# Kernel optimization log

Measured on AMD Instinct MI355X. Metric: run time of the kernel, lower is better.

Reference implementation:

```python
import jax, jax.numpy as jnp
import numpy as np
from jax import lax

silu = jax.nn.silu

def conv2d(x, w, b, pad):
    y = lax.conv_general_dilated(x, w, (1, 1), [(pad, pad), (pad, pad)],
                                 dimension_numbers=('NCHW', 'OIHW', 'NCHW'))
    return y + b[None, :, None, None]

def avgpool2(x):
    B, C, H, W = x.shape
    return x.reshape(B, C, H // 2, 2, W // 2, 2).mean(axis=(3, 5))

def up2x(x):
    # bilinear scale_factor=2, align_corners=True (matches F.interpolate)
    B, C, H, W = x.shape
    Ho, Wo = 2 * H, 2 * W
    ys = jnp.arange(Ho, dtype=x.dtype) * ((H - 1) / (Ho - 1))
    xs = jnp.arange(Wo, dtype=x.dtype) * ((W - 1) / (Wo - 1))
    y0 = jnp.floor(ys).astype(jnp.int32); y1 = jnp.minimum(y0 + 1, H - 1); wy = ys - y0
    x0 = jnp.floor(xs).astype(jnp.int32); x1 = jnp.minimum(x0 + 1, W - 1); wx = xs - x0
    row = x[:, :, y0, :] * (1 - wy)[None, None, :, None] + x[:, :, y1, :] * wy[None, None, :, None]
    return row[:, :, :, x0] * (1 - wx) + row[:, :, :, x1] * wx

def deform_conv2d(x, offset, weight, groups):
    # torchvision DeformConv2d semantics: stride=1, pad=(k-1)//2, dilation=1, no bias
    B, Cin, H, W = x.shape
    Cout, cpg, kh, kw = weight.shape  # cpg = Cin // groups
    K = kh * kw
    OG = offset.shape[1] // (2 * K)   # offset groups
    Cog = Cin // OG
    off = offset.reshape(B, OG, K, 2, H, W)  # (dy, dx) per kernel tap
    ki = jnp.repeat(jnp.arange(kh, dtype=x.dtype) - (kh - 1) // 2, kw)  # [K]
    kj = jnp.tile(jnp.arange(kw, dtype=x.dtype) - (kw - 1) // 2, kh)
    py = off[:, :, :, 0] + jnp.arange(H, dtype=x.dtype)[None, None, None, :, None] + ki[None, None, :, None, None]
    px = off[:, :, :, 1] + jnp.arange(W, dtype=x.dtype)[None, None, None, None, :] + kj[None, None, :, None, None]
    y0f = jnp.floor(py); x0f = jnp.floor(px)
    ly = py - y0f; lx = px - x0f
    y0 = y0f.astype(jnp.int32); x0 = x0f.astype(jnp.int32)
    xg = x.reshape(B, OG, Cog, H * W)

    def corner(yi, xi, wt):
        valid = (yi >= 0) & (yi < H) & (xi >= 0) & (xi < W)
        idx = jnp.clip(yi, 0, H - 1) * W + jnp.clip(xi, 0, W - 1)        # [B,OG,K,H,W]
        idxf = jnp.broadcast_to(idx.reshape(B, OG, 1, K * H * W), (B, OG, Cog, K * H * W))
        v = jnp.take_along_axis(xg, idxf, axis=3).reshape(B, OG, Cog, K, H, W)
        return v * (wt * valid)[:, :, None]

    val = (corner(y0, x0, (1 - ly) * (1 - lx)) + corner(y0, x0 + 1, (1 - ly) * lx)
           + corner(y0 + 1, x0, ly * (1 - lx)) + corner(y0 + 1, x0 + 1, ly * lx))
    # grouped contraction over sampled taps
    valg = val.reshape(B, groups, Cin // groups, K, H, W)
    wg = weight.reshape(groups, Cout // groups, cpg, K)
    return jnp.einsum('bgckhw,gock->bgohw', valg, wg).reshape(B, Cout, H, W)

def setup_inputs() -> dict:
    key = jax.random.key(0)
    ks = iter(jax.random.split(key, 64))
    def w(shape, s=0.05):
        return jax.random.normal(next(ks), shape, jnp.float32) * s
    B, H, W = 4, 512, 512
    d = {'x': jax.random.normal(next(ks), (B, 4, H, W), jnp.float32)}
    # offset estimators (small scale so sampled offsets stay moderate)
    d['eo1_w1'] = w((18, 4, 5, 5), 0.02);  d['eo1_b1'] = w((18,), 0.02)
    d['eo1_w2'] = w((36, 18, 5, 5), 0.02); d['eo1_b2'] = w((36,), 0.02)
    d['dcw1'] = w((2, 2, 3, 3))            # DeformConv2d(4->2, groups=2)
    d['c1d_w1'] = w((4, 2, 3, 3));   d['c1d_b1'] = w((4,))
    d['c1d_w2'] = w((8, 4, 3, 3));   d['c1d_b2'] = w((8,))
    d['eo2_w1'] = w((18, 8, 5, 5), 0.02);  d['eo2_b1'] = w((18,), 0.02)
    d['eo2_w2'] = w((36, 18, 5, 5), 0.02); d['eo2_b2'] = w((36,), 0.02)
    d['dcw2'] = w((8, 4, 3, 3))            # DeformConv2d(8->8, groups=2)
    d['c2d_w1'] = w((12, 8, 3, 3));  d['c2d_b1'] = w((12,))
    d['c2d_w2'] = w((16, 12, 3, 3)); d['c2d_b2'] = w((16,))
    d['eo3_w1'] = w((18, 16, 5, 5), 0.02); d['eo3_b1'] = w((18,), 0.02)
    d['eo3_w2'] = w((36, 18, 5, 5), 0.02); d['eo3_b2'] = w((36,), 0.02)
    d['dcw3'] = w((16, 8, 3, 3))           # DeformConv2d(16->16, groups=2)
    d['c3d_w1'] = w((14, 16, 3, 3)); d['c3d_b1'] = w((14,))
    d['c3d_w2'] = w((12, 14, 3, 3)); d['c3d_b2'] = w((12,))
    d['up2_w'] = w((12, 12, 3, 3));  d['up2_b'] = w((12,))
    d['c2u_w1'] = w((16, 28, 3, 3)); d['c2u_b1'] = w((16,))
    d['c2u_w2'] = w((8, 16, 3, 3));  d['c2u_b2'] = w((8,))
    d['up1_w'] = w((8, 8, 3, 3));    d['up1_b'] = w((8,))
    d['c1u_w1'] = w((8, 16, 3, 3));  d['c1u_b1'] = w((8,))
    d['c1u_w2'] = w((2, 8, 3, 3));   d['c1u_b2'] = w((2,))
    return d

def reference(x, eo1_w1, eo1_b1, eo1_w2, eo1_b2, dcw1, c1d_w1, c1d_b1, c1d_w2, c1d_b2,
              eo2_w1, eo2_b1, eo2_w2, eo2_b2, dcw2, c2d_w1, c2d_b1, c2d_w2, c2d_b2,
              eo3_w1, eo3_b1, eo3_w2, eo3_b2, dcw3, c3d_w1, c3d_b1, c3d_w2, c3d_b2,
              up2_w, up2_b, c2u_w1, c2u_b1, c2u_w2, c2u_b2, up1_w, up1_b,
              c1u_w1, c1u_b1, c1u_w2, c1u_b2):
    def convbasic(h, w1, b1, w2, b2):
        return silu(conv2d(silu(conv2d(h, w1, b1, 1)), w2, b2, 1))
    # level 1 down
    off1 = conv2d(conv2d(x, eo1_w1, eo1_b1, 2), eo1_w2, eo1_b2, 2)
    comp1 = deform_conv2d(x, off1, dcw1, groups=2)
    conv1_d = convbasic(comp1, c1d_w1, c1d_b1, c1d_w2, c1d_b2)
    pool1 = avgpool2(conv1_d)
    # level 2 down
    off2 = conv2d(conv2d(pool1, eo2_w1, eo2_b1, 2), eo2_w2, eo2_b2, 2)
    comp2 = deform_conv2d(pool1, off2, dcw2, groups=2)
    conv2_d = convbasic(comp2, c2d_w1, c2d_b1, c2d_w2, c2d_b2)
    pool2 = avgpool2(conv2_d)
    # level 3 (bottleneck)
    off3 = conv2d(conv2d(pool2, eo3_w1, eo3_b1, 2), eo3_w2, eo3_b2, 2)
    comp3 = deform_conv2d(pool2, off3, dcw3, groups=2)
    conv3_d = convbasic(comp3, c3d_w1, c3d_b1, c3d_w2, c3d_b2)
    # up path
    usmpl2 = silu(conv2d(up2x(conv3_d), up2_w, up2_b, 1))
    conv2_u = convbasic(jnp.concatenate([usmpl2, conv2_d], axis=1), c2u_w1, c2u_b1, c2u_w2, c2u_b2)
    usmpl1 = silu(conv2d(up2x(conv2_u), up1_w, up1_b, 1))
    conv1_u = convbasic(jnp.concatenate([usmpl1, conv1_d], axis=1), c1u_w1, c1u_b1, c1u_w2, c1u_b2)
    return conv1_u
```

## Files before the change

### kernel.cpp

```cpp
#include <hip/hip_runtime.h>
#include <math.h>

#define THREADS 256
typedef __attribute__((ext_vector_type(2))) float f32x2;
typedef __attribute__((ext_vector_type(4))) float f32x4;

__device__ __forceinline__ float silu_f(float v) {
    return v / (1.f + __expf(-v));
}

__device__ __forceinline__ void pk_fma_lo(f32x2& d, f32x2 a, f32x2 b) {
    asm("v_pk_fma_f32 %0, %1, %2, %0 op_sel:[0,0,0] op_sel_hi:[0,1,1]"
        : "+v"(d) : "v"(a), "v"(b));
}
__device__ __forceinline__ void pk_fma_hi(f32x2& d, f32x2 a, f32x2 b) {
    asm("v_pk_fma_f32 %0, %1, %2, %0 op_sel:[1,0,0] op_sel_hi:[1,1,1]"
        : "+v"(d) : "v"(a), "v"(b));
}

struct TEnt { const float* src; int dst; int cin; int cout; int k2; int base; int n; };
struct TTab { TEnt e[40]; int total; };

__global__ __launch_bounds__(THREADS)
void transpose_w_k(TTab t, float* __restrict__ tw) {
    const int i = blockIdx.x * THREADS + threadIdx.x;
    if (i >= t.total) return;
    int j = 0;
    while (i >= t.e[j].base + t.e[j].n) ++j;
    const TEnt e = t.e[j];
    const int local = i - e.base;
    const int co  = local % e.cout;
    const int tmp = local / e.cout;
    const int k   = tmp % e.k2;
    const int ci  = tmp / e.k2;
    tw[e.dst + local] = e.src[(co * e.cin + ci) * e.k2 + k];
}

template<int KS, int PX>
__device__ __forceinline__ void load_row(float* __restrict__ rr,
                                         const float* __restrict__ rp,
                                         bool vy, int x0, int W)
{
    constexpr int PAD = (KS - 1) / 2;
    constexpr int RW = PX + KS - 1;
#pragma unroll
    for (int q = -1; q <= PX / 4; ++q) {
        if (4 * q + 3 + PAD < 0 || 4 * q + PAD >= RW) continue;
        const int xs = x0 + 4 * q;
        constexpr bool SAFE_Q = false;
        (void)SAFE_Q;
        const bool safe = (q >= 0) && (4 * q + 3 < PX);
        float vc[4] = {0.f, 0.f, 0.f, 0.f};
        if (safe) {
            if (vy) {
                const float4 v = *reinterpret_cast<const float4*>(rp + xs);
                vc[0] = v.x; vc[1] = v.y; vc[2] = v.z; vc[3] = v.w;
            }
        } else if (vy && xs >= 0 && xs + 4 <= W) {
            const float4 v = *reinterpret_cast<const float4*>(rp + xs);
            vc[0] = v.x; vc[1] = v.y; vc[2] = v.z; vc[3] = v.w;
        } else if (vy) {
#pragma unroll
            for (int c = 0; c < 4; ++c)
                vc[c] = ((unsigned)(xs + c) < (unsigned)W) ? rp[xs + c] : 0.f;
        }
#pragma unroll
        for (int c = 0; c < 4; ++c) {
            const int t = 4 * q + c + PAD;
            if (t >= 0 && t < RW) rr[t] = vc[c];
        }
    }
}

template<int CIN, int COUT, int KS, int PX, int PHASE, int RW2, int WQ, int NP>
__device__ __forceinline__ void chan_body(
    const float* __restrict__ ip0, const float* __restrict__ sw,
    int cl, int y, int x0, int W, int H, int lw, int total,
    f32x2 (&r2)[2][RW2], f32x4 (&wb)[2][WQ], f32x2 (&acc)[NP][PX])
{
    constexpr int PAD = (KS - 1) / 2;
    constexpr int K2 = KS * KS;
    constexpr int CO_S = (COUT + 3) & ~3;
#pragma unroll
    for (int ky = 0; ky < KS; ++ky) {
        {
            const bool last = (ky + 1 == KS);
            const int ncl = cl + (last ? 1 : 0);
            const int nky = last ? 0 : (ky + 1);
            if (!last || ncl < CIN) {
                const int yy = y + nky - PAD;
                load_row<KS, PX>((float*)r2[(PHASE + ky + 1) & 1],
                                 ip0 + (size_t)ncl * total + (yy << lw),
                                 (unsigned)yy < (unsigned)H, x0, W);
            }
        }
#pragma unroll
        for (int kx = 0; kx < KS; ++kx) {
            const int t = ky * KS + kx;
            const int wc = (PHASE + t) & 1;
            if (t + 1 < K2 || cl + 1 < CIN) {
                const f32x4* __restrict__ nx =
                    (const f32x4*)(sw + (size_t)(cl * K2 + t + 1) * CO_S);
#pragma unroll
                for (int q = 0; q < WQ; ++q) wb[wc ^ 1][q] = nx[q];
            }
#pragma unroll
            for (int q = 0; q < WQ; ++q) {
                const f32x4 w4 = wb[wc][q];
                const f32x2 wlo = __builtin_shufflevector(w4, w4, 0, 1);
                const f32x2 whi = __builtin_shufflevector(w4, w4, 2, 3);
#pragma unroll
                for (int s = 0; s < 2; ++s) {
                    const int p = 2 * q + s;
                    if (p < NP) {
                        const f32x2 wp = s ? whi : wlo;
#pragma unroll
                        for (int j = 0; j < PX; ++j) {
                            const int e = kx + j;
                            if (e & 1) pk_fma_hi(acc[p][j], r2[(PHASE + ky) & 1][e >> 1], wp);
                            else       pk_fma_lo(acc[p][j], r2[(PHASE + ky) & 1][e >> 1], wp);
                        }
                    }
                }
            }
            __builtin_amdgcn_sched_barrier(0);
        }
    }
}

template<int CIN, int COUT, int KS, bool ACT, int PX>
__global__ __launch_bounds__(THREADS)
void conv_sl_k(const float* __restrict__ in, const float* __restrict__ wt,
               const float* __restrict__ bias, float* __restrict__ out,
               int H, int lw, int bs_in, int bs_out, int nb, int nz)
{
    constexpr int PAD = (KS - 1) / 2;
    constexpr int K2 = KS * KS;
    constexpr int CO_S = (COUT + 3) & ~3;
    constexpr int WQ = CO_S / 4;
    constexpr int NP = COUT / 2;
    constexpr int RW = PX + KS - 1;
    constexpr int RW2 = (RW + 1) / 2;
    static_assert(CIN % 2 == 0 && COUT % 2 == 0 && PX % 4 == 0, "");
    __shared__ float sw[CIN * K2 * CO_S];

    const int lin = blockIdx.x;
    const int r8 = lin & 7;
    int q = lin >> 3;
    const int z = q % nz; q /= nz;
    const int g = q * 8 + r8;
    const int b = g % nb;
    const int xb = g / nb;

    const float* __restrict__ wz = wt + (size_t)z * (CIN * K2 * COUT);
    const int W = 1 << lw;
    const int total = H << lw;
    const int idx = (xb * THREADS + threadIdx.x) * PX;
    const float* ip0 = in + (size_t)b * bs_in;
    float* op = out + (size_t)b * bs_out + (size_t)z * COUT * total;
    const int x0 = idx & (W - 1);
    const int y  = idx >> lw;

    for (int i = threadIdx.x; i < CIN * K2 * COUT; i += THREADS)
        sw[(i / COUT) * CO_S + i % COUT] = wz[i];
    __syncthreads();

    f32x2 acc[NP][PX];
#pragma unroll
    for (int p = 0; p < NP; ++p) {
        f32x2 bb;
        bb.x = bias[z * COUT + 2 * p];
        bb.y = bias[z * COUT + 2 * p + 1];
#pragma unroll
        for (int j = 0; j < PX; ++j) acc[p][j] = bb;
    }

    f32x2 r2[2][RW2];
    f32x4 wb[2][WQ];
    {
        const int yy = y - PAD;
        load_row<KS, PX>((float*)r2[0], ip0 + (yy << lw),
                         (unsigned)yy < (unsigned)H, x0, W);
        const f32x4* __restrict__ w0 = (const f32x4*)sw;
#pragma unroll
        for (int q2 = 0; q2 < WQ; ++q2) wb[0][q2] = w0[q2];
    }

#pragma unroll 1
    for (int c2 = 0; c2 < CIN / 2; ++c2) {
        chan_body<CIN, COUT, KS, PX, 0, RW2, WQ, NP>(ip0, sw, 2 * c2,     y, x0, W, H, lw, total, r2, wb, acc);
        chan_body<CIN, COUT, KS, PX, 1, RW2, WQ, NP>(ip0, sw, 2 * c2 + 1, y, x0, W, H, lw, total, r2, wb, acc);
    }

#pragma unroll
    for (int p = 0; p < NP; ++p) {
#pragma unroll
        for (int h = 0; h < 2; ++h) {
            const int co = 2 * p + h;
#pragma unroll
            for (int j4 = 0; j4 < PX / 4; ++j4) {
                float4 v;
                float a0 = h ? acc[p][4 * j4 + 0].y : acc[p][4 * j4 + 0].x;
                float a1 = h ? acc[p][4 * j4 + 1].y : acc[p][4 * j4 + 1].x;
                float a2 = h ? acc[p][4 * j4 + 2].y : acc[p][4 * j4 + 2].x;
                float a3 = h ? acc[p][4 * j4 + 3].y : acc[p][4 * j4 + 3].x;
                v.x = ACT ? silu_f(a0) : a0;
                v.y = ACT ? silu_f(a1) : a1;
                v.z = ACT ? silu_f(a2) : a2;
                v.w = ACT ? silu_f(a3) : a3;
                *reinterpret_cast<float4*>(op + (size_t)co * total + idx + 4 * j4) = v;
            }
        }
    }
}

template<int CIN, int COUT, int KS, bool ACT, int PX>
__global__ __launch_bounds__(THREADS)
void conv_k(const float* __restrict__ in, const float* __restrict__ wt,
            const float* __restrict__ bias, float* __restrict__ out,
            int H, int lw, int bs_in, int bs_out)
{
    constexpr int PAD = (KS - 1) / 2;
    constexpr int K2 = KS * KS;
    constexpr int CO_S = (COUT + 3) & ~3;
    constexpr int WQ = CO_S / 4;
    constexpr int NP = COUT / 2;
    constexpr int RW = PX + KS - 1;
    constexpr int RW2 = (RW + 1) / 2;
    static_assert(COUT % 2 == 0, "");
    __shared__ float sw[CIN * K2 * CO_S];

    const int W = 1 << lw;
    const int total = H << lw;
    const int idx = (blockIdx.x * THREADS + threadIdx.x) * PX;
    const float* ip0 = in + (size_t)blockIdx.y * bs_in;
    float* op = out + (size_t)blockIdx.y * bs_out;
    const int x0 = idx & (W - 1);
    const int y  = idx >> lw;

    for (int i = threadIdx.x; i < CIN * K2 * COUT; i += THREADS)
        sw[(i / COUT) * CO_S + i % COUT] = wt[i];
    __syncthreads();

    f32x2 acc[NP][PX];
#pragma unroll
    for (int p = 0; p < NP; ++p) {
        f32x2 bb;
        bb.x = bias[2 * p];
        bb.y = bias[2 * p + 1];
#pragma unroll
        for (int j = 0; j < PX; ++j) acc[p][j] = bb;
    }

#pragma unroll 1
    for (int cl = 0; cl < CIN; ++cl) {
        const float* __restrict__ row0 = ip0 + (size_t)cl * total;
        f32x2 r2[KS][RW2];
#pragma unroll
        for (int ky = 0; ky < KS; ++ky) {
            const int yy = y + ky - PAD;
            load_row<KS, PX>((float*)r2[ky], row0 + (yy << lw),
                             (unsigned)yy < (unsigned)H, x0, W);
        }
        const float* __restrict__ wbase = &sw[cl * K2 * CO_S];
#pragma unroll
        for (int t = 0; t < K2; ++t) {
            const int ky = t / KS, kx = t % KS;
            const f32x4* __restrict__ wv = (const f32x4*)(wbase + t * CO_S);
#pragma unroll
            for (int q = 0; q < WQ; ++q) {
                const f32x4 w4 = wv[q];
                const f32x2 wlo = __builtin_shufflevector(w4, w4, 0, 1);
                const f32x2 whi = __builtin_shufflevector(w4, w4, 2, 3);
#pragma unroll
                for (int s = 0; s < 2; ++s) {
                    const int p = 2 * q + s;
                    if (p < NP) {
                        const f32x2 wp = s ? whi : wlo;
#pragma unroll
                        for (int j = 0; j < PX; ++j) {
                            const int e = kx + j;
                            if (e & 1) pk_fma_hi(acc[p][j], r2[ky][e >> 1], wp);
                            else       pk_fma_lo(acc[p][j], r2[ky][e >> 1], wp);
                        }
                    }
                }
            }
            __builtin_amdgcn_sched_barrier(0);
        }
    }

#pragma unroll
    for (int p = 0; p < NP; ++p) {
#pragma unroll
        for (int h = 0; h < 2; ++h) {
            const int co = 2 * p + h;
            if (PX == 2) {
                float2 v;
                float a0 = h ? acc[p][0].y : acc[p][0].x;
                float a1 = h ? acc[p][1].y : acc[p][1].x;
                v.x = ACT ? silu_f(a0) : a0;
                v.y = ACT ? silu_f(a1) : a1;
                *reinterpret_cast<float2*>(op + (size_t)co * total + idx) = v;
            } else {
#pragma unroll
                for (int j4 = 0; j4 < PX / 4; ++j4) {
                    float4 v;
                    float a0 = h ? acc[p][4 * j4 + 0].y : acc[p][4 * j4 + 0].x;
                    float a1 = h ? acc[p][4 * j4 + 1].y : acc[p][4 * j4 + 1].x;
                    float a2 = h ? acc[p][4 * j4 + 2].y : acc[p][4 * j4 + 2].x;
                    float a3 = h ? acc[p][4 * j4 + 3].y : acc[p][4 * j4 + 3].x;
                    v.x = ACT ? silu_f(a0) : a0;
                    v.y = ACT ? silu_f(a1) : a1;
                    v.z = ACT ? silu_f(a2) : a2;
                    v.w = ACT ? silu_f(a3) : a3;
                    *reinterpret_cast<float4*>(op + (size_t)co * total + idx + 4 * j4) = v;
                }
            }
        }
    }
}

template<int CIN, int COUT>
__global__ __launch_bounds__(THREADS)
void dconv_k(const float* __restrict__ in, const float* __restrict__ off,
             const float* __restrict__ twg0, const float* __restrict__ twg1,
             float* __restrict__ out,
             int H, int lw, int bs_in, int bs_off, int bs_out)
{
    constexpr int K = 9;
    constexpr int OG = 2;
    constexpr int COG = CIN / OG;
    constexpr int COUTG = COUT / 2;
    constexpr int NWG = COG * K * COUTG;
    __shared__ float sw[2 * NWG];
    for (int i = threadIdx.x; i < 2 * NWG; i += THREADS)
        sw[i] = (i < NWG) ? twg0[i] : twg1[i - NWG];
    __syncthreads();

    const int W = 1 << lw;
    const int total = H << lw;
    const int idx = blockIdx.x * THREADS + threadIdx.x;
    const float* ip0 = in + (size_t)blockIdx.y * bs_in;
    const float* offp = off + (size_t)blockIdx.y * bs_off;
    float* op = out + (size_t)blockIdx.y * bs_out;
    const int x = idx & (W - 1);
    const int y = idx >> lw;

    float acc[COUT];
#pragma unroll
    for (int co = 0; co < COUT; ++co) acc[co] = 0.f;

#pragma unroll
    for (int og = 0; og < OG; ++og) {
#pragma unroll
        for (int k = 0; k < K; ++k) {
            const int ki = k / 3 - 1;
            const int kj = k % 3 - 1;
            const float dy = offp[(size_t)(((og * K + k) * 2 + 0)) * total + idx];
            const float dx = offp[(size_t)(((og * K + k) * 2 + 1)) * total + idx];
            const float py = dy + (float)(y + ki);
            const float px = dx + (float)(x + kj);
            const float y0f = floorf(py), x0f = floorf(px);
            const float ly = py - y0f, lx = px - x0f;
            const int y0 = (int)y0f, x0 = (int)x0f;
            const int y1 = y0 + 1, x1 = x0 + 1;
            const bool vy0 = (unsigned)y0 < (unsigned)H;
            const bool vy1 = (unsigned)y1 < (unsigned)H;
            const bool vx0 = (unsigned)x0 < (unsigned)W;
            const bool vx1 = (unsigned)x1 < (unsigned)W;
            const int cy0 = min(max(y0, 0), H - 1), cy1 = min(max(y1, 0), H - 1);
            const int cx0 = min(max(x0, 0), W - 1), cx1 = min(max(x1, 0), W - 1);
            const int i00 = (cy0 << lw) + cx0, i01 = (cy0 << lw) + cx1;
            const int i10 = (cy1 << lw) + cx0, i11 = (cy1 << lw) + cx1;
            const float f00 = (vy0 && vx0) ? (1.f - ly) * (1.f - lx) : 0.f;
            const float f01 = (vy0 && vx1) ? (1.f - ly) * lx : 0.f;
            const float f10 = (vy1 && vx0) ? ly * (1.f - lx) : 0.f;
            const float f11 = (vy1 && vx1) ? ly * lx : 0.f;
            const float* swg = &sw[og * NWG];
#pragma unroll
            for (int c = 0; c < COG; ++c) {
                const float* __restrict__ ip = ip0 + (size_t)(og * COG + c) * total;
                const float v = f00 * ip[i00] + f01 * ip[i01]
                              + f10 * ip[i10] + f11 * ip[i11];
                const float* __restrict__ wr = &swg[(c * K + k) * COUTG];
#pragma unroll
                for (int col = 0; col < COUTG; ++col)
                    acc[og * COUTG + col] = fmaf(v, wr[col], acc[og * COUTG + col]);
            }
        }
    }

#pragma unroll
    for (int co = 0; co < COUT; ++co)
        op[(size_t)co * total + idx] = acc[co];
}

__global__ __launch_bounds__(THREADS)
void avgpool_k(const float* __restrict__ in, float* __restrict__ out,
               int n, int lt, int lwo, int bsi, int bso)
{
    const int idx = blockIdx.x * THREADS + threadIdx.x;
    if (idx >= n) return;
    const float* ip0 = in + (size_t)blockIdx.y * bsi;
    float* op = out + (size_t)blockIdx.y * bso;
    const int c = idx >> lt;
    const int r = idx & ((1 << lt) - 1);
    const int oy = r >> lwo;
    const int ox = r & ((1 << lwo) - 1);
    const int Wi = 2 << lwo;
    const float* ip = ip0 + ((size_t)c << (lt + 2)) + ((size_t)(2 * oy) << (lwo + 1)) + 2 * ox;
    const float2 t = *reinterpret_cast<const float2*>(ip);
    const float2 b = *reinterpret_cast<const float2*>(ip + Wi);
    op[idx] = 0.25f * (t.x + t.y + b.x + b.y);
}

__global__ __launch_bounds__(THREADS)
void up2x_k(const float* __restrict__ in, float* __restrict__ out,
            int n, int lt, int lwo, int Hin, int bsi, int bso)
{
    const int idx = blockIdx.x * THREADS + threadIdx.x;
    if (idx >= n) return;
    const float* ip0 = in + (size_t)blockIdx.y * bsi;
    float* op = out + (size_t)blockIdx.y * bso;
    const int c = idx >> lt;
    const int r = idx & ((1 << lt) - 1);
    const int oy = r >> lwo;
    const int ox = r & ((1 << lwo) - 1);
    const int W = 1 << (lwo - 1);
    const int H = Hin;
    const float s = (float)(H - 1) / (float)(2 * H - 1);
    const float fy = (float)oy * s;
    const float fx = (float)ox * s;
    const int y0 = (int)fy;
    const int x0 = (int)fx;
    const int y1 = min(y0 + 1, H - 1);
    const int x1 = min(x0 + 1, W - 1);
    const float wy = fy - (float)y0;
    const float wx = fx - (float)x0;
    const float* ip = ip0 + ((size_t)c << (lt - 2));
    const float v00 = ip[y0 * W + x0], v01 = ip[y0 * W + x1];
    const float v10 = ip[y1 * W + x0], v11 = ip[y1 * W + x1];
    op[idx] = (v00 * (1.f - wy) + v10 * wy) * (1.f - wx)
            + (v01 * (1.f - wy) + v11 * wy) * wx;
}

__global__ __launch_bounds__(THREADS)
void copy_k(float4* __restrict__ dst, const float4* __restrict__ src,
            int n4, int bsd, int bss)
{
    const int i = blockIdx.x * THREADS + threadIdx.x;
    if (i >= n4) return;
    dst[(size_t)blockIdx.y * bsd + i] = src[(size_t)blockIdx.y * bss + i];
}


extern "C" void kernel_launch(void* const* d_in, const int* in_sizes, int n_in,
                              void* d_out, int out_size, void* d_ws, size_t ws_size,
                              hipStream_t stream) {
    const float* x      = (const float*)d_in[0];
    const float* eo1_b1 = (const float*)d_in[2];
    const float* eo1_b2 = (const float*)d_in[4];
    const float* c1d_b1 = (const float*)d_in[7];
    const float* c1d_b2 = (const float*)d_in[9];
    const float* eo2_b1 = (const float*)d_in[11];
    const float* eo2_b2 = (const float*)d_in[13];
    const float* c2d_b1 = (const float*)d_in[16];
    const float* c2d_b2 = (const float*)d_in[18];
    const float* eo3_b1 = (const float*)d_in[20];
    const float* eo3_b2 = (const float*)d_in[22];
    const float* c3d_b1 = (const float*)d_in[25];
    const float* c3d_b2 = (const float*)d_in[27];
    const float* up2_b  = (const float*)d_in[29];
    const float* c2u_b1 = (const float*)d_in[31];
    const float* c2u_b2 = (const float*)d_in[33];
    const float* up1_b  = (const float*)d_in[35];
    const float* c1u_b1 = (const float*)d_in[37];
    const float* c1u_b2 = (const float*)d_in[39];

    float* out = (float*)d_out;
    float* wsf = (float*)d_ws;

    constexpr int H1 = 512, A1 = H1 * H1;
    constexpr int H2 = 256, A2 = H2 * H2;
    constexpr int H3 = 128, A3 = H3 * H3;
    constexpr int TW_FLOATS = 81920;
    constexpr int SLOT = 58 * A1;

    const int widx[34]  = {1, 1, 1,  3, 3, 3, 3, 3,  6, 8,
                           10, 10, 10,  12, 12, 12, 12, 12,  15, 17,
                           19,  21, 21, 21, 21, 21,  24, 26,
                           28, 30, 32, 34, 36, 38};
    const int wcin[34]  = {4, 4, 4,  18, 18, 18, 18, 18,  2, 4,
                           8, 8, 8,  18, 18, 18, 18, 18,  8, 12,
                           16,  18, 18, 18, 18, 18,  16, 14,
                           12, 28, 16, 8, 16, 8};
    const int wcout[34] = {6, 6, 6,  8, 8, 8, 8, 4,  4, 8,
                           6, 6, 6,  8, 8, 8, 8, 4,  12, 16,
                           18,  8, 8, 8, 8, 4,  14, 12,
                           12, 16, 8, 8, 8, 2};
    const int wk2[34]   = {25, 25, 25,  25, 25, 25, 25, 25,  9, 9,
                           25, 25, 25,  25, 25, 25, 25, 25,  9, 9,
                           25,  25, 25, 25, 25, 25,  9, 9,
                           9, 9, 9, 9, 9, 9};
    const int wsoff[34] = {0, 600, 1200,  0, 3600, 7200, 10800, 14400,  0, 0,
                           0, 1200, 2400,  0, 3600, 7200, 10800, 14400,  0, 0,
                           0,  0, 3600, 7200, 10800, 14400,  0, 0,
                           0, 0, 0, 0, 0, 0};
    const int cont[34]  = {1, 1, 0,  1, 1, 1, 0, 0,  0, 0,
                           1, 1, 0,  1, 1, 1, 0, 0,  0, 0,
                           0,  1, 1, 1, 0, 0,  0, 0,
                           0, 0, 0, 0, 0, 0};
    TTab tab;
    const float* tw[40];
    int off = 0, base = 0;
    for (int i = 0; i < 34; ++i) {
        const int n = wcin[i] * wcout[i] * wk2[i];
        tab.e[i].src = (const float*)d_in[widx[i]] + wsoff[i];
        tab.e[i].dst = off; tab.e[i].cin = wcin[i]; tab.e[i].cout = wcout[i];
        tab.e[i].k2 = wk2[i]; tab.e[i].base = base; tab.e[i].n = n;
        tw[i] = wsf + off;
        off = cont[i] ? (off + n) : ((off + n + 63) & ~63);
        base += n;
    }
    const int didx[3]   = {5, 14, 23};
    const int dcoutg[3] = {1, 4, 8};
    const int dcpg[3]   = {2, 4, 8};
    for (int i = 0; i < 3; ++i) {
        for (int g = 0; g < 2; ++g) {
            const int e = 34 + 2 * i + g;
            const int n = dcoutg[i] * dcpg[i] * 9;
            tab.e[e].src = (const float*)d_in[didx[i]] + (size_t)g * n;
            tab.e[e].dst = off; tab.e[e].cin = dcpg[i]; tab.e[e].cout = dcoutg[i];
            tab.e[e].k2 = 9; tab.e[e].base = base; tab.e[e].n = n;
            tw[e] = wsf + off;
            off = (off + n + 63) & ~63;
            base += n;
        }
    }
    tab.total = base;
    transpose_w_k<<<(base + THREADS - 1) / THREADS, THREADS, 0, stream>>>(tab, wsf);

    int B = 4;
    while (B > 1 && ws_size < ((size_t)TW_FLOATS + (size_t)B * SLOT) * sizeof(float)) B >>= 1;

    auto run_all = [&](int Bc, float* slot, int SB,
                       const float* xin, int xbs, float* outp, int obs) {
        float* S0 = slot;
        float* S1 = S0 + 36 * A1;
        float* S2 = S1 + 18 * A1;
        float* P  = S2 + 2 * A1;
        float* L1 = S1 + 10 * A1;
        float* L2 = S0 + 32 * A1;
        auto gs = [&](int n, int px, int z) { return dim3((n / (px * THREADS)) * Bc * z); };
        auto gp = [&](int n, int px) { return dim3(n / (px * THREADS), Bc); };
        auto g1 = [&](int n) { return dim3((n + THREADS - 1) / THREADS, Bc); };

        conv_sl_k<4, 6, 5, false, 8><<<gs(A1, 8, 3), THREADS, 0, stream>>>(xin, tw[0], eo1_b1, S1, H1, 9, xbs, SB, Bc, 3);
        conv_sl_k<18, 8, 5, false, 8><<<gs(A1, 8, 4), THREADS, 0, stream>>>(S1, tw[3], eo1_b2, S0, H1, 9, SB, SB, Bc, 4);
        conv_sl_k<18, 4, 5, false, 8><<<gs(A1, 8, 1), THREADS, 0, stream>>>(S1, tw[7], eo1_b2 + 32, S0 + 32 * A1, H1, 9, SB, SB, Bc, 1);
        dconv_k<4, 2><<<g1(A1), THREADS, 0, stream>>>(xin, S0, tw[34], tw[35], S2, H1, 9, xbs, SB, SB);
        conv_k<2, 4, 3, true, 8><<<gp(A1, 8), THREADS, 0, stream>>>(S2, tw[8], c1d_b1, S1, H1, 9, SB, SB);
        conv_k<4, 8, 3, true, 8><<<gp(A1, 8), THREADS, 0, stream>>>(S1, tw[9], c1d_b2, L1, H1, 9, SB, SB);
        avgpool_k<<<g1(8 * A2), THREADS, 0, stream>>>(L1, P, 8 * A2, 16, 8, SB, SB);

        conv_sl_k<8, 6, 5, false, 8><<<gs(A2, 8, 3), THREADS, 0, stream>>>(P, tw[10], eo2_b1, S1, H2, 8, SB, SB, Bc, 3);
        conv_sl_k<18, 8, 5, false, 8><<<gs(A2, 8, 4), THREADS, 0, stream>>>(S1, tw[13], eo2_b2, S0, H2, 8, SB, SB, Bc, 4);
        conv_sl_k<18, 4, 5, false, 8><<<gs(A2, 8, 1), THREADS, 0, stream>>>(S1, tw[17], eo2_b2 + 32, S0 + 32 * A2, H2, 8, SB, SB, Bc, 1);
        dconv_k<8, 8><<<g1(A2), THREADS, 0, stream>>>(P, S0, tw[36], tw[37], S2, H2, 8, SB, SB, SB);
        conv_k<8, 12, 3, true, 4><<<gp(A2, 4), THREADS, 0, stream>>>(S2, tw[18], c2d_b1, S1, H2, 8, SB, SB);
        conv_k<12, 16, 3, true, 4><<<gp(A2, 4), THREADS, 0, stream>>>(S1, tw[19], c2d_b2, L2, H2, 8, SB, SB);
        avgpool_k<<<g1(16 * A3), THREADS, 0, stream>>>(L2, P, 16 * A3, 14, 7, SB, SB);

        conv_k<16, 18, 5, false, 2><<<gp(A3, 2), THREADS, 0, stream>>>(P, tw[20], eo3_b1, S1, H3, 7, SB, SB);
        conv_sl_k<18, 8, 5, false, 4><<<gs(A3, 4, 4), THREADS, 0, stream>>>(S1, tw[21], eo3_b2, S0, H3, 7, SB, SB, Bc, 4);
        conv_sl_k<18, 4, 5, false, 4><<<gs(A3, 4, 1), THREADS, 0, stream>>>(S1, tw[25], eo3_b2 + 32, S0 + 32 * A3, H3, 7, SB, SB, Bc, 1);
        dconv_k<16, 16><<<g1(A3), THREADS, 0, stream>>>(P, S0, tw[38], tw[39], S2, H3, 7, SB, SB, SB);
        conv_k<16, 14, 3, true, 2><<<gp(A3, 2), THREADS, 0, stream>>>(S2, tw[26], c3d_b1, S1, H3, 7, SB, SB);
        conv_k<14, 12, 3, true, 2><<<gp(A3, 2), THREADS, 0, stream>>>(S1, tw[27], c3d_b2, S2, H3, 7, SB, SB);

        up2x_k<<<g1(12 * A2), THREADS, 0, stream>>>(S2, S0, 12 * A2, 16, 8, H3, SB, SB);
        conv_k<12, 12, 3, true, 4><<<gp(A2, 4), THREADS, 0, stream>>>(S0, tw[28], up2_b, S1, H2, 8, SB, SB);
        copy_k<<<g1(4 * A2), THREADS, 0, stream>>>((float4*)(S1 + 12 * A2), (const float4*)L2,
                                                   4 * A2, SB / 4, SB / 4);
        conv_k<28, 16, 3, true, 4><<<gp(A2, 4), THREADS, 0, stream>>>(S1, tw[29], c2u_b1, S0, H2, 8, SB, SB);
        conv_k<16, 8, 3, true, 4><<<gp(A2, 4), THREADS, 0, stream>>>(S0, tw[30], c2u_b2, S2, H2, 8, SB, SB);

        up2x_k<<<g1(8 * A1), THREADS, 0, stream>>>(S2, S0, 8 * A1, 18, 9, H2, SB, SB);
        conv_k<8, 8, 3, true, 8><<<gp(A1, 8), THREADS, 0, stream>>>(S0, tw[31], up1_b, S0 + 8 * A1, H1, 9, SB, SB);
        copy_k<<<g1(2 * A1), THREADS, 0, stream>>>((float4*)(S0 + 16 * A1), (const float4*)L1,
                                                   2 * A1, SB / 4, SB / 4);
        conv_k<16, 8, 3, true, 8><<<gp(A1, 8), THREADS, 0, stream>>>(S0 + 8 * A1, tw[32], c1u_b1, S1, H1, 9, SB, SB);
        conv_k<8, 2, 3, true, 8><<<gp(A1, 8), THREADS, 0, stream>>>(S1, tw[33], c1u_b2, outp, H1, 9, SB, obs);
    };

    for (int g = 0; g < 4; g += B)
        run_all(B, wsf + TW_FLOATS, SLOT,
                x + (size_t)g * 4 * A1, 4 * A1,
                out + (size_t)g * 2 * A1, 2 * A1);
}
```

Measured before the change: 1.536 ms.

## Read conv weights via scalar loads into SGPRs instead of LDS staging

Removes the shared-memory weight staging and __syncthreads from both conv kernels. Weights are now read straight from global memory as uniform values with a double-buffered prefetch, and the packed FMA asm takes the weight operand as an SGPR. This cuts LDS traffic, VGPR pressure and the block-start barrier. In exchange it relies on the compiler emitting scalar loads and on the scalar cache holding the weights, and if it does not, the inline asm 's' constraints could force readfirstlane moves or fail to compile.

```diff
diff --git a/kernel.cpp b/kernel.cpp
--- a/kernel.cpp
+++ b/kernel.cpp
@@ -3,19 +3,18 @@
 
 #define THREADS 256
 typedef __attribute__((ext_vector_type(2))) float f32x2;
-typedef __attribute__((ext_vector_type(4))) float f32x4;
 
 __device__ __forceinline__ float silu_f(float v) {
     return v / (1.f + __expf(-v));
 }
 
-__device__ __forceinline__ void pk_fma_lo(f32x2& d, f32x2 a, f32x2 b) {
+__device__ __forceinline__ void pk_fma_lo_s(f32x2& d, f32x2 a, f32x2 b) {
     asm("v_pk_fma_f32 %0, %1, %2, %0 op_sel:[0,0,0] op_sel_hi:[0,1,1]"
-        : "+v"(d) : "v"(a), "v"(b));
-}
-__device__ __forceinline__ void pk_fma_hi(f32x2& d, f32x2 a, f32x2 b) {
+        : "+v"(d) : "v"(a), "s"(b));
+}
+__device__ __forceinline__ void pk_fma_hi_s(f32x2& d, f32x2 a, f32x2 b) {
     asm("v_pk_fma_f32 %0, %1, %2, %0 op_sel:[1,0,0] op_sel_hi:[1,1,1]"
-        : "+v"(d) : "v"(a), "v"(b));
+        : "+v"(d) : "v"(a), "s"(b));
 }
 
 struct TEnt { const float* src; int dst; int cin; int cout; int k2; int base; int n; };
@@ -47,8 +46,6 @@
     for (int q = -1; q <= PX / 4; ++q) {
         if (4 * q + 3 + PAD < 0 || 4 * q + PAD >= RW) continue;
         const int xs = x0 + 4 * q;
-        constexpr bool SAFE_Q = false;
-        (void)SAFE_Q;
         const bool safe = (q >= 0) && (4 * q + 3 < PX);
         float vc[4] = {0.f, 0.f, 0.f, 0.f};
         if (safe) {
@@ -72,15 +69,15 @@
     }
 }
 
-template<int CIN, int COUT, int KS, int PX, int PHASE, int RW2, int WQ, int NP>
+template<int CIN, int COUT, int KS, int PX, int PHASE, int RW2, int NP>
 __device__ __forceinline__ void chan_body(
-    const float* __restrict__ ip0, const float* __restrict__ sw,
+    const float* __restrict__ ip0, const float* __restrict__ wz,
     int cl, int y, int x0, int W, int H, int lw, int total,
-    f32x2 (&r2)[2][RW2], f32x4 (&wb)[2][WQ], f32x2 (&acc)[NP][PX])
+    f32x2 (&r2)[2][RW2], f32x2 (&wb)[2][NP], f32x2 (&acc)[NP][PX])
 {
     constexpr int PAD = (KS - 1) / 2;
     constexpr int K2 = KS * KS;
-    constexpr int CO_S = (COUT + 3) & ~3;
+    static_assert(K2 % 2 == 1, "parity continuity needs odd K2");
 #pragma unroll
     for (int ky = 0; ky < KS; ++ky) {
         {
@@ -99,28 +96,19 @@
             const int t = ky * KS + kx;
             const int wc = (PHASE + t) & 1;
             if (t + 1 < K2 || cl + 1 < CIN) {
-                const f32x4* __restrict__ nx =
-                    (const f32x4*)(sw + (size_t)(cl * K2 + t + 1) * CO_S);
-#pragma unroll
-                for (int q = 0; q < WQ; ++q) wb[wc ^ 1][q] = nx[q];
-            }
-#pragma unroll
-            for (int q = 0; q < WQ; ++q) {
-                const f32x4 w4 = wb[wc][q];
-                const f32x2 wlo = __builtin_shufflevector(w4, w4, 0, 1);
-                const f32x2 whi = __builtin_shufflevector(w4, w4, 2, 3);
-#pragma unroll
-                for (int s = 0; s < 2; ++s) {
-                    const int p = 2 * q + s;
-                    if (p < NP) {
-                        const f32x2 wp = s ? whi : wlo;
-#pragma unroll
-                        for (int j = 0; j < PX; ++j) {
-                            const int e = kx + j;
-                            if (e & 1) pk_fma_hi(acc[p][j], r2[(PHASE + ky) & 1][e >> 1], wp);
-                            else       pk_fma_lo(acc[p][j], r2[(PHASE + ky) & 1][e >> 1], wp);
-                        }
-                    }
+                const f32x2* __restrict__ nx =
+                    (const f32x2*)(wz + (size_t)(cl * K2 + t + 1) * COUT);
+#pragma unroll
+                for (int p = 0; p < NP; ++p) wb[wc ^ 1][p] = nx[p];
+            }
+#pragma unroll
+            for (int p = 0; p < NP; ++p) {
+                const f32x2 wp = wb[wc][p];
+#pragma unroll
+                for (int j = 0; j < PX; ++j) {
+                    const int e = kx + j;
+                    if (e & 1) pk_fma_hi_s(acc[p][j], r2[(PHASE + ky) & 1][e >> 1], wp);
+                    else       pk_fma_lo_s(acc[p][j], r2[(PHASE + ky) & 1][e >> 1], wp);
                 }
             }
             __builtin_amdgcn_sched_barrier(0);
@@ -136,13 +124,10 @@
 {
     constexpr int PAD = (KS - 1) / 2;
     constexpr int K2 = KS * KS;
-    constexpr int CO_S = (COUT + 3) & ~3;
-    constexpr int WQ = CO_S / 4;
     constexpr int NP = COUT / 2;
     constexpr int RW = PX + KS - 1;
     constexpr int RW2 = (RW + 1) / 2;
     static_assert(CIN % 2 == 0 && COUT % 2 == 0 && PX % 4 == 0, "");
-    __shared__ float sw[CIN * K2 * CO_S];
 
     const int lin = blockIdx.x;
     const int r8 = lin & 7;
@@ -161,10 +146,6 @@
     const int x0 = idx & (W - 1);
     const int y  = idx >> lw;
 
-    for (int i = threadIdx.x; i < CIN * K2 * COUT; i += THREADS)
-        sw[(i / COUT) * CO_S + i % COUT] = wz[i];
-    __syncthreads();
-
     f32x2 acc[NP][PX];
 #pragma unroll
     for (int p = 0; p < NP; ++p) {
@@ -176,20 +157,20 @@
     }
 
     f32x2 r2[2][RW2];
-    f32x4 wb[2][WQ];
+    f32x2 wb[2][NP];
     {
         const int yy = y - PAD;
         load_row<KS, PX>((float*)r2[0], ip0 + (yy << lw),
                          (unsigned)yy < (unsigned)H, x0, W);
-        const f32x4* __restrict__ w0 = (const f32x4*)sw;
-#pragma unroll
-        for (int q2 = 0; q2 < WQ; ++q2) wb[0][q2] = w0[q2];
+        const f32x2* __restrict__ w0 = (const f32x2*)wz;
+#pragma unroll
+        for (int p = 0; p < NP; ++p) wb[0][p] = w0[p];
     }
 
 #pragma unroll 1
     for (int c2 = 0; c2 < CIN / 2; ++c2) {
-        chan_body<CIN, COUT, KS, PX, 0, RW2, WQ, NP>(ip0, sw, 2 * c2,     y, x0, W, H, lw, total, r2, wb, acc);
-        chan_body<CIN, COUT, KS, PX, 1, RW2, WQ, NP>(ip0, sw, 2 * c2 + 1, y, x0, W, H, lw, total, r2, wb, acc);
+        chan_body<CIN, COUT, KS, PX, 0, RW2, NP>(ip0, wz, 2 * c2,     y, x0, W, H, lw, total, r2, wb, acc);
+        chan_body<CIN, COUT, KS, PX, 1, RW2, NP>(ip0, wz, 2 * c2 + 1, y, x0, W, H, lw, total, r2, wb, acc);
     }
 
 #pragma unroll
@@ -222,13 +203,10 @@
 {
     constexpr int PAD = (KS - 1) / 2;
     constexpr int K2 = KS * KS;
-    constexpr int CO_S = (COUT + 3) & ~3;
-    constexpr int WQ = CO_S / 4;
     constexpr int NP = COUT / 2;
     constexpr int RW = PX + KS - 1;
     constexpr int RW2 = (RW + 1) / 2;
     static_assert(COUT % 2 == 0, "");
-    __shared__ float sw[CIN * K2 * CO_S];
 
     const int W = 1 << lw;
     const int total = H << lw;
@@ -238,10 +216,6 @@
     const int x0 = idx & (W - 1);
     const int y  = idx >> lw;
 
-    for (int i = threadIdx.x; i < CIN * K2 * COUT; i += THREADS)
-        sw[(i / COUT) * CO_S + i % COUT] = wt[i];
-    __syncthreads();
-
     f32x2 acc[NP][PX];
 #pragma unroll
     for (int p = 0; p < NP; ++p) {
@@ -262,28 +236,29 @@
             load_row<KS, PX>((float*)r2[ky], row0 + (yy << lw),
                              (unsigned)yy < (unsigned)H, x0, W);
         }
-        const float* __restrict__ wbase = &sw[cl * K2 * CO_S];
+        const float* __restrict__ wc0 = wt + (size_t)cl * K2 * COUT;
+        f32x2 wb[2][NP];
+        {
+            const f32x2* __restrict__ w0 = (const f32x2*)wc0;
+#pragma unroll
+            for (int p = 0; p < NP; ++p) wb[0][p] = w0[p];
+        }
 #pragma unroll
         for (int t = 0; t < K2; ++t) {
             const int ky = t / KS, kx = t % KS;
-            const f32x4* __restrict__ wv = (const f32x4*)(wbase + t * CO_S);
-#pragma unroll
-            for (int q = 0; q < WQ; ++q) {
-                const f32x4 w4 = wv[q];
-                const f32x2 wlo = __builtin_shufflevector(w4, w4, 0, 1);
-                const f32x2 whi = __builtin_shufflevector(w4, w4, 2, 3);
-#pragma unroll
-                for (int s = 0; s < 2; ++s) {
-                    const int p = 2 * q + s;
-                    if (p < NP) {
-                        const f32x2 wp = s ? whi : wlo;
-#pragma unroll
-                        for (int j = 0; j < PX; ++j) {
-                            const int e = kx + j;
-                            if (e & 1) pk_fma_hi(acc[p][j], r2[ky][e >> 1], wp);
-                            else       pk_fma_lo(acc[p][j], r2[ky][e >> 1], wp);
-                        }
-                    }
+            if (t + 1 < K2) {
+                const f32x2* __restrict__ nx = (const f32x2*)(wc0 + (t + 1) * COUT);
+#pragma unroll
+                for (int p = 0; p < NP; ++p) wb[(t + 1) & 1][p] = nx[p];
+            }
+#pragma unroll
+            for (int p = 0; p < NP; ++p) {
+                const f32x2 wp = wb[t & 1][p];
+#pragma unroll
+                for (int j = 0; j < PX; ++j) {
+                    const int e = kx + j;
+                    if (e & 1) pk_fma_hi_s(acc[p][j], r2[ky][e >> 1], wp);
+                    else       pk_fma_lo_s(acc[p][j], r2[ky][e >> 1], wp);
                 }
             }
             __builtin_amdgcn_sched_barrier(0);
```

New measurement: 1.619 ms. 1.05x slower.
